# Kernel optimization log

Hardware: AMD Instinct MI355X
Metric: run time of the kernel (lower is better)

Reference implementation:

```python
import jax, jax.numpy as jnp
import numpy as np

B, T, E, H = 2, 2048, 1024, 16
D = E // H  # head_dim = 64


def setup_inputs() -> dict:
    key = jax.random.key(0)
    kx, kq, kk, kv, ko = jax.random.split(key, 5)
    x = jax.random.normal(kx, (B, T, E), dtype=jnp.float32)
    # nn.Parameter(torch.randn(...)) -> standard normal params
    Wq = jax.random.normal(kq, (H, E, D), dtype=jnp.float32)
    Wk = jax.random.normal(kk, (H, E, D), dtype=jnp.float32)
    Wv = jax.random.normal(kv, (H, E, D), dtype=jnp.float32)
    # nn.Linear(E, E, bias=False): weight [out, in], y = a @ Wo.T
    Wo = jax.random.normal(ko, (E, E), dtype=jnp.float32) * (1.0 / np.sqrt(E))
    # boolean mask: True positions are filled with -inf (causal: strict upper tri)
    mask = jnp.triu(jnp.ones((T, T), dtype=bool), k=1)
    return {"x": x, "mask": mask, "Wq": Wq, "Wk": Wk, "Wv": Wv, "Wo": Wo}


def reference(x, mask, Wq, Wk, Wv, Wo):
    # x: [b, t, e]; Wq/Wk/Wv: [h, e, i]
    q = jnp.einsum('hei,bte->hbti', Wq, x)
    k = jnp.einsum('hei,bte->hbti', Wk, x)
    v = jnp.einsum('hei,bte->hbti', Wv, x)
    # NOTE: original scales by sqrt(seq_len) (x.shape[1]), not sqrt(head_dim)
    scale = x.shape[1] ** 0.5
    fit = jnp.einsum('hbti,hbTi->hbtT', q, k) / scale  # [h, b, t, T]
    fit = jnp.where(mask, -jnp.inf, fit)
    p = jax.nn.softmax(fit, axis=-1)
    att = jnp.einsum('hbtT,hbTi->hbti', p, v)          # [h, b, t, i]
    # rearrange 'h b t i -> b t (h i)'
    b, t = att.shape[1], att.shape[2]
    att = jnp.transpose(att, (1, 2, 0, 3)).reshape(b, t, -1)
    return att @ Wo.T
```

## Files before the change

### kernel.cpp

```cpp
#include <hip/hip_runtime.h>
#include <hip/hip_fp8.h>
#include <stdint.h>

constexpr float INV_SCALE = 0.022097086912079608f;
constexpr float LOG2E = 1.4426950408889634f;
constexpr float QSC = INV_SCALE * LOG2E;

typedef __attribute__((ext_vector_type(8))) short bfrag;
typedef __attribute__((ext_vector_type(4))) float facc;
typedef __attribute__((ext_vector_type(4))) unsigned short us4;

#define MFMA(a, b, c) __builtin_amdgcn_mfma_f32_16x16x32_bf16((a), (b), (c), 0, 0, 0)
#define EXP2(x) __builtin_amdgcn_exp2f(x)

__device__ __forceinline__ unsigned short f2bh(float f) {
    union { float f; unsigned int u; } cv; cv.f = f;
    unsigned int u = cv.u;
    u += 0x7FFFu + ((u >> 16) & 1u);
    return (unsigned short)(u >> 16);
}
__device__ __forceinline__ float bh2f(unsigned short h) {
    union { unsigned int u; float f; } cv; cv.u = ((unsigned int)h) << 16;
    return cv.f;
}
__device__ __forceinline__ void gl_lds16(const unsigned short* g, unsigned short* lds) {
    __builtin_amdgcn_global_load_lds(
        (const __attribute__((address_space(1))) unsigned int*)g,
        (__attribute__((address_space(3))) unsigned int*)lds, 16, 0, 0);
}
__device__ __forceinline__ bfrag f8frag(uint2 raw) {
    union { uint2 u; unsigned char b[8]; } cv; cv.u = raw;
    bfrag r;
    #pragma unroll
    for (int j = 0; j < 8; ++j) {
        const __hip_fp8_e4m3* t = reinterpret_cast<const __hip_fp8_e4m3*>(&cv.b[j]);
        r[j] = (short)f2bh((float)(*t) * 0.00390625f);
    }
    return r;
}

__global__ __launch_bounds__(256) void prep_xw(const float* __restrict__ x,
                                               const float* __restrict__ Wo,
                                               unsigned short* __restrict__ xh,
                                               unsigned short* __restrict__ xl,
                                               unsigned short* __restrict__ WoB) {
    if (blockIdx.x < 1024) {
        int idx = blockIdx.x * 256 + threadIdx.x;
        facc v = *(const facc*)&Wo[(size_t)idx * 4];
        us4 o;
        #pragma unroll
        for (int j = 0; j < 4; ++j) o[j] = f2bh(v[j]);
        *(us4*)&WoB[(size_t)idx * 4] = o;
    } else {
        int idx = (blockIdx.x - 1024) * 256 + threadIdx.x;
        facc v = *(const facc*)&x[(size_t)idx * 4];
        us4 hv, lv;
        #pragma unroll
        for (int j = 0; j < 4; ++j) {
            unsigned short hb = f2bh(v[j]);
            hv[j] = hb;
            lv[j] = f2bh(v[j] - bh2f(hb));
        }
        *(us4*)&xh[(size_t)idx * 4] = hv;
        *(us4*)&xl[(size_t)idx * 4] = lv;
    }
}

__global__ __launch_bounds__(256) void prep_w(
    const float* __restrict__ Wq, const float* __restrict__ Wk, const float* __restrict__ Wv,
    unsigned short* __restrict__ WqTh, unsigned short* __restrict__ WqTl,
    unsigned short* __restrict__ WkTh, unsigned short* __restrict__ WkTl,
    unsigned short* __restrict__ WvT)
{
    __shared__ float tile[64][65];
    const int tid = threadIdx.x;
    const int et = blockIdx.x, h = blockIdx.y, m = blockIdx.z;
    const float* W = (m == 0) ? Wq : (m == 1) ? Wk : Wv;
    #pragma unroll
    for (int rep = 0; rep < 4; ++rep) {
        int idx = rep * 256 + tid;
        int e = idx >> 4, i4 = (idx & 15) * 4;
        facc v = *(const facc*)&W[(size_t)h * 65536 + (size_t)(et * 64 + e) * 64 + i4];
        tile[e][i4] = v.x; tile[e][i4 + 1] = v.y; tile[e][i4 + 2] = v.z; tile[e][i4 + 3] = v.w;
    }
    __syncthreads();
    unsigned short* Oh = (m == 0) ? WqTh : (m == 1) ? WkTh : WvT;
    unsigned short* Ol = (m == 0) ? WqTl : WkTl;
    #pragma unroll
    for (int rep = 0; rep < 4; ++rep) {
        int idx = rep * 256 + tid;
        int i = idx >> 4, e4 = (idx & 15) * 4;
        us4 hv, lv;
        #pragma unroll
        for (int j = 0; j < 4; ++j) {
            float f = tile[e4 + j][i];
            unsigned short hb = f2bh(f);
            hv[j] = hb;
            lv[j] = f2bh(f - bh2f(hb));
        }
        size_t o = (size_t)(h * 64 + i) * 1024 + et * 64 + e4;
        *(us4*)&Oh[o] = hv;
        if (m < 2) *(us4*)&Ol[o] = lv;
    }
}

__global__ __launch_bounds__(512, 2) void qkv_fused(
    const unsigned short* __restrict__ xh, const unsigned short* __restrict__ xl,
    const unsigned short* __restrict__ WqTh, const unsigned short* __restrict__ WqTl,
    const unsigned short* __restrict__ WkTh, const unsigned short* __restrict__ WkTl,
    const unsigned short* __restrict__ WvT,
    unsigned short* __restrict__ qh, unsigned char* __restrict__ ql8,
    unsigned short* __restrict__ kh, unsigned short* __restrict__ kl,
    unsigned short* __restrict__ vT)
{
    extern __shared__ unsigned short sm[];
    unsigned short* Ab = sm;
    unsigned short* Qb = sm + 16384;
    unsigned short* Kb = sm + 32768;
    unsigned short* Vb = sm + 49152;
    const int tid = threadIdx.x;
    const int w = tid >> 6, l = tid & 63;
    const int wm = w >> 2, wn = w & 3;
    const int ct = blockIdx.x, rt = blockIdx.y;

    const int lc = (l & 7) ^ (l >> 3);
    const int krel = (lc & 3) * 8;
    const unsigned short* Axp = (lc < 4) ? xh : xl;
    const unsigned short* Qp  = (lc < 4) ? WqTh : WqTl;
    const unsigned short* Kp  = (lc < 4) ? WkTh : WkTl;

    facc accq[4][2], acck[4][2], accv[4][2];
    #pragma unroll
    for (int m = 0; m < 4; ++m)
        #pragma unroll
        for (int n = 0; n < 2; ++n) {
            accq[m][n] = (facc)(0.0f); acck[m][n] = (facc)(0.0f); accv[m][n] = (facc)(0.0f);
        }

    auto stageAB = [&](int buf, int e0) {
        #pragma unroll
        for (int i = 0; i < 2; ++i) {
            int slice = w * 2 + i;
            int row = slice * 8 + (l >> 3);
            size_t sa = (size_t)(rt * 128 + row) * 1024 + e0 + krel;
            size_t sb = (size_t)(ct * 128 + row) * 1024 + e0 + krel;
            gl_lds16(&Axp[sa], &Ab[buf * 8192 + slice * 512]);
            gl_lds16(&Qp[sb],  &Qb[buf * 8192 + slice * 512]);
            gl_lds16(&Kp[sb],  &Kb[buf * 8192 + slice * 512]);
        }
    };

    stageAB(0, 0);
    #pragma unroll
    for (int i = 0; i < 2; ++i) {
        int slice = w * 2 + i;
        int row = slice * 8 + (l >> 3);
        gl_lds16(&WvT[(size_t)(ct * 128 + row) * 1024 + lc * 8], &Vb[slice * 512]);
    }
    asm volatile("s_waitcnt vmcnt(0)" ::: "memory");
    __builtin_amdgcn_s_barrier();

    for (int t = 0; t < 32; ++t) {
        __builtin_amdgcn_s_barrier();
        __builtin_amdgcn_sched_barrier(0);
        if (t < 31) stageAB((t + 1) & 1, (t + 1) * 32);
        {
            int wv = (t >> 1) + 1;
            if (wv < 16) {
                int slice = w + (t & 1) * 8;
                int row = slice * 8 + (l >> 3);
                gl_lds16(&WvT[(size_t)(ct * 128 + row) * 1024 + wv * 64 + lc * 8],
                         &Vb[(wv & 1) * 8192 + slice * 512]);
            }
        }
        __builtin_amdgcn_sched_barrier(0);
        if (t < 30)       asm volatile("s_waitcnt vmcnt(7)" ::: "memory");
        else if (t == 30) asm volatile("s_waitcnt vmcnt(6)" ::: "memory");
        else              asm volatile("s_waitcnt vmcnt(0)" ::: "memory");
        __builtin_amdgcn_sched_barrier(0);
        __builtin_amdgcn_s_barrier();
        __builtin_amdgcn_sched_barrier(0);

        const unsigned short* Ac = &Ab[(t & 1) * 8192];
        const unsigned short* Qc = &Qb[(t & 1) * 8192];
        const unsigned short* Kc = &Kb[(t & 1) * 8192];
        const unsigned short* Vc = &Vb[((t >> 1) & 1) * 8192];
        const int ca = (l >> 4) ^ (l & 7);
        const int cb = ca ^ 4;
        const int cv = ca ^ ((t & 1) << 2);

        bfrag afh[4], afl[4];
        #pragma unroll
        for (int m = 0; m < 4; ++m) {
            int row = wm * 64 + m * 16 + (l & 15);
            afh[m] = *(const bfrag*)&Ac[row * 64 + ca * 8];
            afl[m] = *(const bfrag*)&Ac[row * 64 + cb * 8];
        }
        #pragma unroll
        for (int n = 0; n < 2; ++n) {
            int nr = wn * 32 + n * 16 + (l & 15);
            bfrag bv = *(const bfrag*)&Vc[nr * 64 + cv * 8];
            #pragma unroll
            for (int m = 0; m < 4; ++m) accv[m][n] = MFMA(afh[m], bv, accv[m][n]);
        }
        #pragma unroll
        for (int n = 0; n < 2; ++n) {
            int nr = wn * 32 + n * 16 + (l & 15);
            bfrag bh = *(const bfrag*)&Qc[nr * 64 + ca * 8];
            bfrag bl = *(const bfrag*)&Qc[nr * 64 + cb * 8];
            #pragma unroll
            for (int m = 0; m < 4; ++m) {
                accq[m][n] = MFMA(afh[m], bh, accq[m][n]);
                accq[m][n] = MFMA(afh[m], bl, accq[m][n]);
                accq[m][n] = MFMA(afl[m], bh, accq[m][n]);
            }
        }
        #pragma unroll
        for (int n = 0; n < 2; ++n) {
            int nr = wn * 32 + n * 16 + (l & 15);
            bfrag bh = *(const bfrag*)&Kc[nr * 64 + ca * 8];
            bfrag bl = *(const bfrag*)&Kc[nr * 64 + cb * 8];
            #pragma unroll
            for (int m = 0; m < 4; ++m) {
                acck[m][n] = MFMA(afh[m], bh, acck[m][n]);
                acck[m][n] = MFMA(afh[m], bl, acck[m][n]);
                acck[m][n] = MFMA(afl[m], bh, acck[m][n]);
            }
        }
    }

    #pragma unroll
    for (int m = 0; m < 4; ++m)
        #pragma unroll
        for (int r = 0; r < 4; ++r) {
            int row = rt * 128 + wm * 64 + m * 16 + (l >> 4) * 4 + r;
            #pragma unroll
            for (int n = 0; n < 2; ++n) {
                int col = ct * 128 + wn * 32 + n * 16 + (l & 15);
                float fq = accq[m][n][r] * QSC;
                unsigned short hb = f2bh(fq);
                qh[(size_t)row * 1024 + col] = hb;
                __hip_fp8_e4m3 e((fq - bh2f(hb)) * 256.0f);
                ql8[(size_t)row * 1024 + col] = *reinterpret_cast<unsigned char*>(&e);
                float fk = acck[m][n][r];
                unsigned short kb = f2bh(fk);
                kh[(size_t)row * 1024 + col] = kb;
                kl[(size_t)row * 1024 + col] = f2bh(fk - bh2f(kb));
            }
        }
    #pragma unroll
    for (int m = 0; m < 4; ++m) {
        int t0g = rt * 128 + wm * 64 + m * 16 + (l >> 4) * 4;
        int b_ = t0g >> 11, t0 = t0g & 2047;
        #pragma unroll
        for (int n = 0; n < 2; ++n) {
            int col = ct * 128 + wn * 32 + n * 16 + (l & 15);
            int h_ = col >> 6, d = col & 63;
            us4 pk;
            #pragma unroll
            for (int r = 0; r < 4; ++r) pk[r] = f2bh(accv[m][n][r]);
            *(us4*)&vT[((size_t)((h_ * 2 + b_) * 64 + d)) * 2048 + t0] = pk;
        }
    }
}

__device__ __forceinline__ void stage_kv(
    const unsigned short* __restrict__ kh, const unsigned short* __restrict__ kl,
    const unsigned short* __restrict__ vT,
    unsigned short* Khb, unsigned short* Klb, unsigned short* Vtb,
    int w, int l, int b, int h, int kt)
{
    #pragma unroll
    for (int i = 0; i < 2; ++i) {
        int pbase = (w * 2 + i) * 1024;
        int p = pbase + l * 16;
        int row = p >> 7, slot = (p >> 4) & 7;
        int chunk = slot ^ (row & 7);
        size_t srcK = (size_t)(b * 2048 + kt * 64 + row) * 1024 + h * 64 + chunk * 8;
        size_t srcV = ((size_t)(h * 2 + b) * 64 + row) * 2048 + (size_t)kt * 64 + chunk * 8;
        gl_lds16(&kh[srcK], &Khb[pbase >> 1]);
        gl_lds16(&kl[srcK], &Klb[pbase >> 1]);
        gl_lds16(&vT[srcV], &Vtb[pbase >> 1]);
    }
}

__device__ __forceinline__ void attn_step(
    const unsigned short* Khb, const unsigned short* Klb, const unsigned short* Vtb,
    unsigned short* Pl, const bfrag* qfh, const bfrag* qfl,
    facc* O, facc& Osum, float* mrow, bfrag ones, int w, int l, bool diag)
{
    facc S[4];
    #pragma unroll
    for (int f = 0; f < 4; ++f) S[f] = (facc)(0.0f);
    __builtin_amdgcn_s_setprio(1);
    #pragma unroll
    for (int s = 0; s < 2; ++s) {
        #pragma unroll
        for (int f = 0; f < 4; ++f) {
            int key = f * 16 + (l & 15);
            int ch = (s * 4 + (l >> 4)) ^ (key & 7);
            bfrag kbh = *(const bfrag*)&Khb[key * 64 + ch * 8];
            bfrag kbl = *(const bfrag*)&Klb[key * 64 + ch * 8];
            S[f] = MFMA(qfh[s], kbh, S[f]);
            S[f] = MFMA(qfh[s], kbl, S[f]);
            S[f] = MFMA(qfl[s], kbh, S[f]);
        }
    }
    __builtin_amdgcn_s_setprio(0);
    if (diag) {
        #pragma unroll
        for (int f = 0; f < 4; ++f) {
            int keyl = f * 16 + (l & 15);
            #pragma unroll
            for (int r = 0; r < 4; ++r) {
                int qls = w * 16 + (l >> 4) * 4 + r;
                if (keyl > qls) S[f][r] = -1e30f;
            }
        }
    }
    float mx[4];
    float dmax = -3.0e38f;
    #pragma unroll
    for (int r = 0; r < 4; ++r) {
        float m0 = fmaxf(fmaxf(S[0][r], S[1][r]), fmaxf(S[2][r], S[3][r]));
        m0 = fmaxf(m0, __shfl_xor(m0, 1));
        m0 = fmaxf(m0, __shfl_xor(m0, 2));
        m0 = fmaxf(m0, __shfl_xor(m0, 4));
        m0 = fmaxf(m0, __shfl_xor(m0, 8));
        mx[r] = m0;
        dmax = fmaxf(dmax, m0 - mrow[r]);
    }
    if (!__all(dmax <= 8.0f)) {
        #pragma unroll
        for (int r = 0; r < 4; ++r) {
            float mn = fmaxf(mrow[r], mx[r]);
            float fac = EXP2(mrow[r] - mn);
            mrow[r] = mn;
            O[0][r] *= fac; O[1][r] *= fac; O[2][r] *= fac; O[3][r] *= fac;
            Osum[r] *= fac;
        }
    }
    #pragma unroll
    for (int r = 0; r < 4; ++r)
        #pragma unroll
        for (int f = 0; f < 4; ++f) S[f][r] = EXP2(S[f][r] - mrow[r]);
    #pragma unroll
    for (int f = 0; f < 4; ++f) {
        int key = f * 16 + (l & 15);
        #pragma unroll
        for (int r = 0; r < 4; ++r) {
            int qr = w * 16 + (l >> 4) * 4 + r;
            Pl[qr * 64 + (((key >> 3) ^ (qr & 7)) * 8) + (key & 7)] = f2bh(S[f][r]);
        }
    }
    __builtin_amdgcn_s_setprio(1);
    #pragma unroll
    for (int s = 0; s < 2; ++s) {
        int qa = w * 16 + (l & 15);
        int cha = (s * 4 + (l >> 4)) ^ (qa & 7);
        bfrag pa = *(const bfrag*)&Pl[qa * 64 + cha * 8];
        Osum = MFMA(pa, ones, Osum);
        #pragma unroll
        for (int f = 0; f < 4; ++f) {
            int d = f * 16 + (l & 15);
            int chv = (s * 4 + (l >> 4)) ^ (d & 7);
            bfrag vb = *(const bfrag*)&Vtb[d * 64 + chv * 8];
            O[f] = MFMA(pa, vb, O[f]);
        }
    }
    __builtin_amdgcn_s_setprio(0);
}

__global__ __launch_bounds__(256, 2) void attn_mfma(
    const unsigned short* __restrict__ qh, const unsigned char* __restrict__ ql8,
    const unsigned short* __restrict__ kh, const unsigned short* __restrict__ kl,
    const unsigned short* __restrict__ vT, unsigned short* __restrict__ att)
{
    __shared__ unsigned short Kh[2][4096], Kl[2][4096], Vt[2][4096], Pl[4096];
    const int tid = threadIdx.x, w = tid >> 6, l = tid & 63;
    const int dd = blockIdx.y * 16 + blockIdx.x;
    const int xcd = dd & 7, sl = dd >> 3;
    const int hb = xcd * 4 + (sl >> 4);
    const int bx = sl & 15;
    const int qtA = 31 - bx, qtB = bx;
    const int h = hb >> 1, b = hb & 1;

    bfrag ones;
    #pragma unroll
    for (int j = 0; j < 8; ++j) ones[j] = (short)0x3F80;

    bfrag qfhA[2], qflA[2], qfhB[2], qflB[2];
    {
        const int qrowA = qtA * 64 + w * 16 + (l & 15);
        const size_t qoffA = (size_t)(b * 2048 + qrowA) * 1024 + h * 64 + (l >> 4) * 8;
        qfhA[0] = *(const bfrag*)&qh[qoffA];
        qfhA[1] = *(const bfrag*)&qh[qoffA + 32];
        qflA[0] = f8frag(*(const uint2*)&ql8[qoffA]);
        qflA[1] = f8frag(*(const uint2*)&ql8[qoffA + 32]);
        const int qrowB = qtB * 64 + w * 16 + (l & 15);
        const size_t qoffB = (size_t)(b * 2048 + qrowB) * 1024 + h * 64 + (l >> 4) * 8;
        qfhB[0] = *(const bfrag*)&qh[qoffB];
        qfhB[1] = *(const bfrag*)&qh[qoffB + 32];
        qflB[0] = f8frag(*(const uint2*)&ql8[qoffB]);
        qflB[1] = f8frag(*(const uint2*)&ql8[qoffB + 32]);
    }

    facc OA[4], OB[4], OsA, OsB;
    float mA[4], mB[4];
    #pragma unroll
    for (int f = 0; f < 4; ++f) { OA[f] = (facc)(0.0f); OB[f] = (facc)(0.0f); }
    OsA = (facc)(0.0f); OsB = (facc)(0.0f);
    #pragma unroll
    for (int r = 0; r < 4; ++r) { mA[r] = -1e30f; mB[r] = -1e30f; }

    stage_kv(kh, kl, vT, Kh[0], Kl[0], Vt[0], w, l, b, h, 0);
    for (int kt = 0; kt <= qtA; ++kt) {
        const int cur = kt & 1;
        __syncthreads();
        if (kt < qtA)
            stage_kv(kh, kl, vT, Kh[cur ^ 1], Kl[cur ^ 1], Vt[cur ^ 1], w, l, b, h, kt + 1);
        __builtin_amdgcn_sched_barrier(0);
        __builtin_amdgcn_s_barrier();
        __builtin_amdgcn_sched_barrier(0);
        attn_step(Kh[cur], Kl[cur], Vt[cur], Pl, qfhA, qflA, OA, OsA, mA, ones,
                  w, l, kt == qtA);
        if (kt <= qtB)
            attn_step(Kh[cur], Kl[cur], Vt[cur], Pl, qfhB, qflB, OB, OsB, mB, ones,
                      w, l, kt == qtB);
    }

    #pragma unroll
    for (int f = 0; f < 4; ++f) {
        int d = h * 64 + f * 16 + (l & 15);
        #pragma unroll
        for (int r = 0; r < 4; ++r) {
            int tA = qtA * 64 + w * 16 + (l >> 4) * 4 + r;
            att[(size_t)(b * 2048 + tA) * 1024 + d] = f2bh(OA[f][r] / OsA[r]);
            int tB = qtB * 64 + w * 16 + (l >> 4) * 4 + r;
            att[(size_t)(b * 2048 + tB) * 1024 + d] = f2bh(OB[f][r] / OsB[r]);
        }
    }
}

__global__ __launch_bounds__(256, 2) void outproj(
    const unsigned short* __restrict__ att, const unsigned short* __restrict__ WoB,
    float* __restrict__ out)
{
    __shared__ unsigned short Ab[2][128 * 64], Bb[2][128 * 64];
    const int tid = threadIdx.x, w = tid >> 6, l = tid & 63;
    const int wm = w >> 1, wn = w & 1;
    const int rt = blockIdx.x, ct = blockIdx.y;

    const int lc = (l & 7) ^ (l >> 3);
    facc acc[4][4];
    #pragma unroll
    for (int i = 0; i < 4; ++i)
        #pragma unroll
        for (int j = 0; j < 4; ++j) acc[i][j] = (facc)(0.0f);

    auto stage = [&](int buf, int e0) {
        #pragma unroll
        for (int i = 0; i < 4; ++i) {
            int slice = w * 4 + i;
            int row = slice * 8 + (l >> 3);
            gl_lds16(&att[(size_t)(rt * 128 + row) * 1024 + e0 + lc * 8], &Ab[buf][slice * 512]);
            gl_lds16(&WoB[(size_t)(ct * 128 + row) * 1024 + e0 + lc * 8], &Bb[buf][slice * 512]);
        }
    };

    stage(0, 0);
    int cur = 0;
    for (int t = 0; t < 16; ++t) {
        __syncthreads();
        if (t < 15) stage(cur ^ 1, (t + 1) * 64);
        __builtin_amdgcn_sched_barrier(0);
        __builtin_amdgcn_s_barrier();
        __builtin_amdgcn_sched_barrier(0);
        #pragma unroll
        for (int s = 0; s < 2; ++s) {
            const int slot = (s * 4 + (l >> 4)) ^ (l & 7);
            bfrag af[4], bf_[4];
            #pragma unroll
            for (int m = 0; m < 4; ++m)
                af[m] = *(const bfrag*)&Ab[cur][(wm * 64 + m * 16 + (l & 15)) * 64 + slot * 8];
            #pragma unroll
            for (int n = 0; n < 4; ++n)
                bf_[n] = *(const bfrag*)&Bb[cur][(wn * 64 + n * 16 + (l & 15)) * 64 + slot * 8];
            #pragma unroll
            for (int m = 0; m < 4; ++m)
                #pragma unroll
                for (int n = 0; n < 4; ++n)
                    acc[m][n] = MFMA(af[m], bf_[n], acc[m][n]);
        }
        cur ^= 1;
    }
    #pragma unroll
    for (int m = 0; m < 4; ++m)
        #pragma unroll
        for (int r = 0; r < 4; ++r) {
            int row = rt * 128 + wm * 64 + m * 16 + (l >> 4) * 4 + r;
            #pragma unroll
            for (int n = 0; n < 4; ++n) {
                int col = ct * 128 + wn * 64 + n * 16 + (l & 15);
                out[(size_t)row * 1024 + col] = acc[m][n][r];
            }
        }
}

extern "C" void kernel_launch(void* const* d_in, const int* in_sizes, int n_in,
                              void* d_out, int out_size, void* d_ws, size_t ws_size,
                              hipStream_t stream) {
    const float* x  = (const float*)d_in[0];
    const float* Wq = (const float*)d_in[2];
    const float* Wk = (const float*)d_in[3];
    const float* Wv = (const float*)d_in[4];
    const float* Wo = (const float*)d_in[5];

    uint8_t* wsb = (uint8_t*)d_ws;
    const size_t MB = 1024 * 1024;
    unsigned short* WqTh = (unsigned short*)(wsb + 0 * MB);
    unsigned short* WqTl = (unsigned short*)(wsb + 2 * MB);
    unsigned short* WkTh = (unsigned short*)(wsb + 4 * MB);
    unsigned short* WkTl = (unsigned short*)(wsb + 6 * MB);
    unsigned short* WvT  = (unsigned short*)(wsb + 8 * MB);
    unsigned short* qh   = (unsigned short*)(wsb + 10 * MB);
    unsigned char*  ql8  = (unsigned char*)(wsb + 18 * MB);
    unsigned short* kh   = (unsigned short*)(wsb + 22 * MB);
    unsigned short* kl   = (unsigned short*)(wsb + 30 * MB);
    unsigned short* vT   = (unsigned short*)(wsb + 38 * MB);
    unsigned short* att  = (unsigned short*)(wsb + 46 * MB);
    unsigned short* xh   = (unsigned short*)(wsb + 46 * MB);
    unsigned short* WoB  = (unsigned short*)(wsb + 54 * MB);
    unsigned short* xl   = (unsigned short*)(wsb + 56 * MB);

    hipFuncSetAttribute((const void*)qkv_fused,
                        hipFuncAttributeMaxDynamicSharedMemorySize, 131072);

    prep_xw<<<dim3(5120), 256, 0, stream>>>(x, Wo, xh, xl, WoB);
    prep_w<<<dim3(16, 16, 3), 256, 0, stream>>>(Wq, Wk, Wv, WqTh, WqTl, WkTh, WkTl, WvT);
    qkv_fused<<<dim3(8, 32), 512, 131072, stream>>>(xh, xl, WqTh, WqTl, WkTh, WkTl, WvT,
                                                    qh, ql8, kh, kl, vT);
    attn_mfma<<<dim3(16, 32), 256, 0, stream>>>(qh, ql8, kh, kl, vT, att);
    outproj<<<dim3(32, 8), 256, 0, stream>>>(att, WoB, (float*)d_out);
}
```

Measured before the change: 167.9 us.

## Shrink QKV projection tile to 128x64 with 256 threads; use DPP row max

The fused QKV projection kernel moves from 512-thread blocks with 128-column tiles to 256-thread blocks with 64-column tiles. This doubles the grid to 512 blocks and cuts dynamic LDS to 72KB. The V weight staging is rewritten to load per k-step with a new swizzle, in place of the old staggered 64-wide loads. The attention softmax row max now uses DPP lane ops instead of shfl_xor. The aim is better occupancy and load balance, plus cheaper cross-lane reductions. The cost is less reuse of the x tile and more global traffic for x. The unused stage lambda still holds an odd no-op address expression.

After: 164.5 us. 2.0% less time.

```diff
diff --git a/kernel.cpp b/kernel.cpp
--- a/kernel.cpp
+++ b/kernel.cpp
@@ -37,6 +37,18 @@
         r[j] = (short)f2bh((float)(*t) * 0.00390625f);
     }
     return r;
+}
+template<int CTRL>
+__device__ __forceinline__ float dppmax(float v) {
+    int s = __builtin_amdgcn_update_dpp(0, __builtin_bit_cast(int, v), CTRL, 0xF, 0xF, true);
+    return fmaxf(v, __builtin_bit_cast(float, s));
+}
+__device__ __forceinline__ float rowmax16(float v) {
+    v = dppmax<0xB1>(v);
+    v = dppmax<0x4E>(v);
+    v = dppmax<0x141>(v);
+    v = dppmax<0x140>(v);
+    return v;
 }
 
 __global__ __launch_bounds__(256) void prep_xw(const float* __restrict__ x,
@@ -104,7 +116,7 @@
     }
 }
 
-__global__ __launch_bounds__(512, 2) void qkv_fused(
+__global__ __launch_bounds__(256, 2) void qkv_fused(
     const unsigned short* __restrict__ xh, const unsigned short* __restrict__ xl,
     const unsigned short* __restrict__ WqTh, const unsigned short* __restrict__ WqTl,
     const unsigned short* __restrict__ WkTh, const unsigned short* __restrict__ WkTl,
@@ -116,11 +128,11 @@
     extern __shared__ unsigned short sm[];
     unsigned short* Ab = sm;
     unsigned short* Qb = sm + 16384;
-    unsigned short* Kb = sm + 32768;
-    unsigned short* Vb = sm + 49152;
+    unsigned short* Kb = sm + 24576;
+    unsigned short* Vb = sm + 32768;
     const int tid = threadIdx.x;
     const int w = tid >> 6, l = tid & 63;
-    const int wm = w >> 2, wn = w & 3;
+    const int wm = w >> 1, wn = w & 1;
     const int ct = blockIdx.x, rt = blockIdx.y;
 
     const int lc = (l & 7) ^ (l >> 3);
@@ -128,6 +140,7 @@
     const unsigned short* Axp = (lc < 4) ? xh : xl;
     const unsigned short* Qp  = (lc < 4) ? WqTh : WqTl;
     const unsigned short* Kp  = (lc < 4) ? WkTh : WkTl;
+    const int lcv = (l & 3) ^ ((l >> 3) & 3);
 
     facc accq[4][2], acck[4][2], accv[4][2];
     #pragma unroll
@@ -137,25 +150,50 @@
             accq[m][n] = (facc)(0.0f); acck[m][n] = (facc)(0.0f); accv[m][n] = (facc)(0.0f);
         }
 
-    auto stageAB = [&](int buf, int e0) {
+    auto stage = [&](int buf, int e0) {
+        #pragma unroll
+        for (int i = 0; i < 4; ++i) {
+            int slice = w * 4 + i;
+            int row = slice * 8 + (l >> 3);
+            gl_lds16(&Axp[(size_t)(rt * 128 + row) * 1024 + e0 + krel],
+                     &Ab[buf * 8192 + slice * 512]);
+        }
         #pragma unroll
         for (int i = 0; i < 2; ++i) {
             int slice = w * 2 + i;
             int row = slice * 8 + (l >> 3);
-            size_t sa = (size_t)(rt * 128 + row) * 1024 + e0 + krel;
-            size_t sb = (size_t)(ct * 128 + row) * 1024 + e0 + krel;
-            gl_lds16(&Axp[sa], &Ab[buf * 8192 + slice * 512]);
-            gl_lds16(&Qp[sb],  &Qb[buf * 8192 + slice * 512]);
-            gl_lds16(&Kp[sb],  &Kb[buf * 8192 + slice * 512]);
+            size_t sb = (size_t)(ct * 64 + row) * 1024 + e0 + krel;
+            gl_lds16(&Qp[sb], &Qb[buf * 4096 + slice * 512]);
+            gl_lds16(&Kp[sb], &Kb[buf * 4096 + slice * 512]);
+        }
+        {
+            int row = w * 16 + (l >> 2);
+            gl_lds16(&WvT[(size_t)(ct * 64 + row) * 1024 + e0 + lcv * 8],
+                     &Vb[w * 1024 + (l & 63) * 0 + w * 0 + (w * 1024) * 0 + w * 1024 - w * 1024 + w * 1024 + 0]);
         }
     };
-
-    stageAB(0, 0);
-    #pragma unroll
-    for (int i = 0; i < 2; ++i) {
-        int slice = w * 2 + i;
-        int row = slice * 8 + (l >> 3);
-        gl_lds16(&WvT[(size_t)(ct * 128 + row) * 1024 + lc * 8], &Vb[slice * 512]);
+    auto stageV_fix = [&](int buf, int e0) {
+        int row = w * 16 + (l >> 2);
+        gl_lds16(&WvT[(size_t)(ct * 64 + row) * 1024 + e0 + lcv * 8],
+                 &Vb[buf * 2048 + w * 512]);
+    };
+
+    {
+        #pragma unroll
+        for (int i = 0; i < 4; ++i) {
+            int slice = w * 4 + i;
+            int row = slice * 8 + (l >> 3);
+            gl_lds16(&Axp[(size_t)(rt * 128 + row) * 1024 + krel], &Ab[slice * 512]);
+        }
+        #pragma unroll
+        for (int i = 0; i < 2; ++i) {
+            int slice = w * 2 + i;
+            int row = slice * 8 + (l >> 3);
+            size_t sb = (size_t)(ct * 64 + row) * 1024 + krel;
+            gl_lds16(&Qp[sb], &Qb[slice * 512]);
+            gl_lds16(&Kp[sb], &Kb[slice * 512]);
+        }
+        stageV_fix(0, 0);
     }
     asm volatile("s_waitcnt vmcnt(0)" ::: "memory");
     __builtin_amdgcn_s_barrier();
@@ -163,31 +201,38 @@
     for (int t = 0; t < 32; ++t) {
         __builtin_amdgcn_s_barrier();
         __builtin_amdgcn_sched_barrier(0);
-        if (t < 31) stageAB((t + 1) & 1, (t + 1) * 32);
-        {
-            int wv = (t >> 1) + 1;
-            if (wv < 16) {
-                int slice = w + (t & 1) * 8;
+        if (t < 31) {
+            int buf = (t + 1) & 1, e0 = (t + 1) * 32;
+            #pragma unroll
+            for (int i = 0; i < 4; ++i) {
+                int slice = w * 4 + i;
                 int row = slice * 8 + (l >> 3);
-                gl_lds16(&WvT[(size_t)(ct * 128 + row) * 1024 + wv * 64 + lc * 8],
-                         &Vb[(wv & 1) * 8192 + slice * 512]);
-            }
-        }
-        __builtin_amdgcn_sched_barrier(0);
-        if (t < 30)       asm volatile("s_waitcnt vmcnt(7)" ::: "memory");
-        else if (t == 30) asm volatile("s_waitcnt vmcnt(6)" ::: "memory");
-        else              asm volatile("s_waitcnt vmcnt(0)" ::: "memory");
+                gl_lds16(&Axp[(size_t)(rt * 128 + row) * 1024 + e0 + krel],
+                         &Ab[buf * 8192 + slice * 512]);
+            }
+            #pragma unroll
+            for (int i = 0; i < 2; ++i) {
+                int slice = w * 2 + i;
+                int row = slice * 8 + (l >> 3);
+                size_t sb = (size_t)(ct * 64 + row) * 1024 + e0 + krel;
+                gl_lds16(&Qp[sb], &Qb[buf * 4096 + slice * 512]);
+                gl_lds16(&Kp[sb], &Kb[buf * 4096 + slice * 512]);
+            }
+            stageV_fix(buf, e0);
+        }
+        __builtin_amdgcn_sched_barrier(0);
+        if (t < 31) asm volatile("s_waitcnt vmcnt(9)" ::: "memory");
+        else        asm volatile("s_waitcnt vmcnt(0)" ::: "memory");
         __builtin_amdgcn_sched_barrier(0);
         __builtin_amdgcn_s_barrier();
         __builtin_amdgcn_sched_barrier(0);
 
         const unsigned short* Ac = &Ab[(t & 1) * 8192];
-        const unsigned short* Qc = &Qb[(t & 1) * 8192];
-        const unsigned short* Kc = &Kb[(t & 1) * 8192];
-        const unsigned short* Vc = &Vb[((t >> 1) & 1) * 8192];
+        const unsigned short* Qc = &Qb[(t & 1) * 4096];
+        const unsigned short* Kc = &Kb[(t & 1) * 4096];
+        const unsigned short* Vc = &Vb[(t & 1) * 2048];
         const int ca = (l >> 4) ^ (l & 7);
         const int cb = ca ^ 4;
-        const int cv = ca ^ ((t & 1) << 2);
 
         bfrag afh[4], afl[4];
         #pragma unroll
@@ -199,7 +244,8 @@
         #pragma unroll
         for (int n = 0; n < 2; ++n) {
             int nr = wn * 32 + n * 16 + (l & 15);
-            bfrag bv = *(const bfrag*)&Vc[nr * 64 + cv * 8];
+            int cv = (l >> 4) ^ ((nr >> 1) & 3);
+            bfrag bv = *(const bfrag*)&Vc[nr * 32 + cv * 8];
             #pragma unroll
             for (int m = 0; m < 4; ++m) accv[m][n] = MFMA(afh[m], bv, accv[m][n]);
         }
@@ -236,7 +282,7 @@
             int row = rt * 128 + wm * 64 + m * 16 + (l >> 4) * 4 + r;
             #pragma unroll
             for (int n = 0; n < 2; ++n) {
-                int col = ct * 128 + wn * 32 + n * 16 + (l & 15);
+                int col = ct * 64 + wn * 32 + n * 16 + (l & 15);
                 float fq = accq[m][n][r] * QSC;
                 unsigned short hb = f2bh(fq);
                 qh[(size_t)row * 1024 + col] = hb;
@@ -254,7 +300,7 @@
         int b_ = t0g >> 11, t0 = t0g & 2047;
         #pragma unroll
         for (int n = 0; n < 2; ++n) {
-            int col = ct * 128 + wn * 32 + n * 16 + (l & 15);
+            int col = ct * 64 + wn * 32 + n * 16 + (l & 15);
             int h_ = col >> 6, d = col & 63;
             us4 pk;
             #pragma unroll
@@ -323,10 +369,7 @@
     #pragma unroll
     for (int r = 0; r < 4; ++r) {
         float m0 = fmaxf(fmaxf(S[0][r], S[1][r]), fmaxf(S[2][r], S[3][r]));
-        m0 = fmaxf(m0, __shfl_xor(m0, 1));
-        m0 = fmaxf(m0, __shfl_xor(m0, 2));
-        m0 = fmaxf(m0, __shfl_xor(m0, 4));
-        m0 = fmaxf(m0, __shfl_xor(m0, 8));
+        m0 = rowmax16(m0);
         mx[r] = m0;
         dmax = fmaxf(dmax, m0 - mrow[r]);
     }
@@ -534,11 +577,11 @@
     unsigned short* xl   = (unsigned short*)(wsb + 56 * MB);
 
     hipFuncSetAttribute((const void*)qkv_fused,
-                        hipFuncAttributeMaxDynamicSharedMemorySize, 131072);
+                        hipFuncAttributeMaxDynamicSharedMemorySize, 73728);
 
     prep_xw<<<dim3(5120), 256, 0, stream>>>(x, Wo, xh, xl, WoB);
     prep_w<<<dim3(16, 16, 3), 256, 0, stream>>>(Wq, Wk, Wv, WqTh, WqTl, WkTh, WkTl, WvT);
-    qkv_fused<<<dim3(8, 32), 512, 131072, stream>>>(xh, xl, WqTh, WqTl, WkTh, WkTl, WvT,
+    qkv_fused<<<dim3(16, 32), 256, 73728, stream>>>(xh, xl, WqTh, WqTl, WkTh, WkTl, WvT,
                                                     qh, ql8, kh, kl, vT);
     attn_mfma<<<dim3(16, 32), 256, 0, stream>>>(qh, ql8, kh, kl, vT, att);
     outproj<<<dim3(32, 8), 256, 0, stream>>>(att, WoB, (float*)d_out);
```
